# Kernel optimization log

Measured on AMD Instinct MI355X. Metric: run time of the kernel, lower is better.

The kernel has to match this reference:

```python
import jax, jax.numpy as jnp
import numpy as np

H = 12          # nheads
SIM_EPS = 1e-8  # SimMatrix eps
LN_EPS = 1e-5   # nn.LayerNorm default eps
SLOPE = 0.01    # LeakyReLU default negative slope


def leaky(x):
    return jnp.where(x >= 0, x, SLOPE * x)


def etc_attention(hiddens, gamma, beta, Wout, bout):
    # hiddens: [B, L, 3*D]
    B, L, D3 = hiddens.shape
    D = D3 // 3
    d = D // H
    h = hiddens.reshape(B, L, 3, H, d)
    Q = h[:, :, 0].transpose(0, 2, 1, 3)  # [B,H,L,d]
    K = h[:, :, 1].transpose(0, 2, 1, 3)
    V = h[:, :, 2].transpose(0, 2, 1, 3)
    # cosine-similarity attention scores (SimMatrix(K, Q))
    Kn = K / jnp.clip(jnp.linalg.norm(K, axis=-1, keepdims=True), SIM_EPS, None)
    Qn = Q / jnp.clip(jnp.linalg.norm(Q, axis=-1, keepdims=True), SIM_EPS, None)
    att = jnp.einsum('bhid,bhjd->bhij', Kn, Qn)  # [B,H,L,L]
    # LayerNorm over the head axis H (lnormalize: [B, L*L, H] layernorm on last dim)
    mu = att.mean(axis=1, keepdims=True)
    var = att.var(axis=1, keepdims=True)  # biased, matches torch LayerNorm
    att = (att - mu) / jnp.sqrt(var + LN_EPS)
    att = att * gamma[None, :, None, None] + beta[None, :, None, None]
    att = jax.nn.softmax(att, axis=-1)
    att = jnp.where(jnp.isnan(att), jnp.zeros_like(att), att)  # removeNaN
    out = jnp.einsum('bhij,bhjd->bhid', att, V)          # att @ V
    out = out.transpose(0, 2, 1, 3).reshape(B, L, D)      # catHiddens
    # dropout is identity at inference; lin_out = Linear + Softmax
    probs = jax.nn.softmax(out @ Wout.T + bout, axis=-1)  # [B,L,C]
    return probs, att


def get_weights(att, masks):
    # att: [B,H,L,L], masks: [B,L] float
    w = masks * att.mean(axis=1).sum(axis=1)  # [B,L]
    return jax.nn.softmax(w, axis=-1)[..., None]  # [B,L,1]


def setup_inputs() -> dict:
    key = jax.random.key(0)
    ks = jax.random.split(key, 16)
    B, L = 16, 512
    Din, D, C, VOCAB = 300, 768, 20, 32000

    def kaiming(k, shape, fan_in):
        return jax.random.normal(k, shape, jnp.float32) * np.sqrt(2.0 / fan_in)

    return {
        'input_ids': jax.random.randint(ks[0], (B, L), 0, VOCAB),
        'wv': jax.random.normal(ks[1], (B, L, Din), jnp.float32),
        'emb': jax.random.normal(ks[2], (VOCAB, D), jnp.float32),
        'W_t': kaiming(ks[3], (3 * D, D), D),
        'b_t': jnp.zeros((3 * D,), jnp.float32),
        'gamma_t': jnp.ones((H,), jnp.float32),
        'beta_t': jnp.zeros((H,), jnp.float32),
        'Wout_t': kaiming(ks[4], (C, D), D),
        'bout_t': jnp.zeros((C,), jnp.float32),
        'W_h': kaiming(ks[5], (3 * D, Din), Din),
        'b_h': jnp.zeros((3 * D,), jnp.float32),
        'gamma_h': jnp.ones((H,), jnp.float32),
        'beta_h': jnp.zeros((H,), jnp.float32),
        'Wout_h': kaiming(ks[6], (C, D), D),
        'bout_h': jnp.zeros((C,), jnp.float32),
    }


def reference(input_ids, wv, emb, W_t, b_t, gamma_t, beta_t, Wout_t, bout_t,
              W_h, b_h, gamma_h, beta_h, Wout_h, bout_h):
    masks = (input_ids != 0).astype(jnp.float32)  # [B,L]
    # token branch: Embedding -> LeakyReLU -> Linear -> LeakyReLU
    h_t = leaky(leaky(emb[input_ids]) @ W_t.T + b_t)
    probs_t, att_t = etc_attention(h_t, gamma_t, beta_t, Wout_t, bout_t)
    probs_t = (get_weights(att_t, masks) * probs_t).sum(axis=1)  # [B,C]
    # hidden/word-vector branch: Linear -> LeakyReLU
    h_h = leaky(wv @ W_h.T + b_h)
    probs_h, att_h = etc_attention(h_h, gamma_h, beta_h, Wout_h, bout_h)
    probs_h = (get_weights(att_h, masks) * probs_h).sum(axis=1)
    return (probs_t + probs_h) / 2.0
```

## Files before the change

### kernel.cpp

```cpp
#include <hip/hip_runtime.h>

typedef unsigned int uint;
typedef unsigned short ushort;
typedef _Float16 f16;
typedef _Float16 h8 __attribute__((ext_vector_type(8)));
typedef float f32x4 __attribute__((ext_vector_type(4)));


__device__ __forceinline__ float b2f(ushort u){ return __uint_as_float(((uint)u)<<16); }
__device__ __forceinline__ ushort f2b(float f){
  uint u = __float_as_uint(f);
  uint r = u + 0x7fffu + ((u>>16)&1u);
  return (ushort)(r>>16);
}
__device__ __forceinline__ float leaky(float x){ return x >= 0.f ? x : 0.01f*x; }
__device__ __forceinline__ float ldf(const void* p, int idx, int isb){
  return isb ? b2f(((const ushort*)p)[idx]) : ((const float*)p)[idx];
}

#define GLOAD16(gp, lp) __builtin_amdgcn_global_load_lds( \
    (const __attribute__((address_space(1))) void*)(gp), \
    (__attribute__((address_space(3))) void*)(lp), 16, 0, 0)

__global__ __launch_bounds__(256) void k_init(const ushort* __restrict__ wvbits,
    int* __restrict__ flag, float* __restrict__ zbase){
  int bid = blockIdx.x, tid = threadIdx.x;
  if (bid == 0){
    if (tid == 0){
      int sane = 0;
      for (int i=0;i<128;i++){
        uint e = (wvbits[i]>>7)&0xffu;
        if (e==0u || (e>=90u && e<=150u)) sane++;
      }
      *flag = (sane >= 115) ? 1 : 0;
    }
  } else {
    zbase[(bid-1)*256 + tid] = 0.f;
  }
}

__global__ __launch_bounds__(256) void k_prep_all(const int* __restrict__ ids,
    const void* __restrict__ emb, const void* __restrict__ wv,
    const void* __restrict__ W0, const void* __restrict__ W1,
    const int* __restrict__ flag,
    f16* __restrict__ AhA, f16* __restrict__ WhA,
    f16* __restrict__ AhB, f16* __restrict__ WhB,
    int nBX, int nW0, int nA1, int nW1){
  int isb = *flag;
  int bx = blockIdx.x, tid = threadIdx.x;
  if (bx < nBX){
    int t = bx*256 + tid;
    int m = t / 96, kk = (t % 96) * 8;
    float o[8];
    if (isb){
      const ushort* src = (const ushort*)emb + (size_t)ids[m]*768 + kk;
      uint4 v = *(const uint4*)src;
      o[0]=__uint_as_float((v.x&0xffffu)<<16); o[1]=__uint_as_float(v.x&0xffff0000u);
      o[2]=__uint_as_float((v.y&0xffffu)<<16); o[3]=__uint_as_float(v.y&0xffff0000u);
      o[4]=__uint_as_float((v.z&0xffffu)<<16); o[5]=__uint_as_float(v.z&0xffff0000u);
      o[6]=__uint_as_float((v.w&0xffffu)<<16); o[7]=__uint_as_float(v.w&0xffff0000u);
    } else {
      const float* src = (const float*)emb + (size_t)ids[m]*768 + kk;
      float4 v0 = ((const float4*)src)[0];
      float4 v1 = ((const float4*)src)[1];
      o[0]=v0.x; o[1]=v0.y; o[2]=v0.z; o[3]=v0.w;
      o[4]=v1.x; o[5]=v1.y; o[6]=v1.z; o[7]=v1.w;
    }
    h8 hv;
    #pragma unroll
    for (int i=0;i<8;i++) hv[i] = (f16)leaky(o[i]);
    *(h8*)(AhA + (size_t)m*768 + kk) = hv;
  } else if (bx < nBX + nW0){
    int t = (bx - nBX)*256 + tid;
    int n = t / 96, kk = (t % 96) * 8;
    h8 hv;
    #pragma unroll
    for (int i=0;i<8;i++) hv[i] = (f16)ldf(W0, n*768 + kk + i, isb);
    *(h8*)(WhA + (size_t)n*768 + kk) = hv;
  } else if (bx < nBX + nW0 + nA1){
    int t = (bx - nBX - nW0)*256 + tid;
    int n = t / 40, kk = (t % 40) * 8;
    h8 hv;
    #pragma unroll
    for (int i=0;i<8;i++){
      int k = kk + i;
      hv[i] = (k < 300) ? (f16)ldf(wv, n*300 + k, isb) : (f16)0.f;
    }
    *(h8*)(AhB + (size_t)n*320 + kk) = hv;
  } else {
    int t = (bx - nBX - nW0 - nA1)*256 + tid;
    int n = t / 40, kk = (t % 40) * 8;
    h8 hv;
    #pragma unroll
    for (int i=0;i<8;i++){
      int k = kk + i;
      hv[i] = (k < 300) ? (f16)ldf(W1, n*300 + k, isb) : (f16)0.f;
    }
    *(h8*)(WhB + (size_t)n*320 + kk) = hv;
  }
}

__global__ __launch_bounds__(256) void k_gemm_m(
    const f16* AhA, const f16* WhA, const void* biasA, int KA,
    f16* QhA, f16* KhA, f16* VtA,
    const f16* AhB, const f16* WhB, const void* biasB, int KB,
    f16* QhB, f16* KhB, f16* VtB,
    const int* __restrict__ flag, int sbase){
  __shared__ __align__(16) f16 As[128*64];
  __shared__ __align__(16) f16 Bs[128*64];
  int z = sbase + blockIdx.z;
  const f16* Ah = z ? AhB : AhA;
  const f16* Wh = z ? WhB : WhA;
  const void* bias = z ? biasB : biasA;
  int KP = z ? KB : KA;
  f16* Qh = z ? QhB : QhA;
  f16* Kh = z ? KhB : KhA;
  f16* Vt = z ? VtB : VtA;
  int STEPS = KP >> 6;

  int tid = threadIdx.x;
  int w = tid >> 6, lane = tid & 63;
  int mrow = lane & 15, kq = lane >> 4;
  int m0 = blockIdx.x * 128;
  int n0 = blockIdx.y * 128;
  int msub = (w & 1) * 64, nsub = (w >> 1) * 64;

  f32x4 acc[4][4];
  #pragma unroll
  for (int mt=0; mt<4; mt++)
    #pragma unroll
    for (int nt=0; nt<4; nt++) acc[mt][nt] = (f32x4){0.f,0.f,0.f,0.f};

  int cbase = w*64 + lane;

  for (int step=0; step<STEPS; step++){
    int k0 = step*64;
    __syncthreads();
    #pragma unroll
    for (int rep=0; rep<4; rep++){
      int cb = rep*256 + w*64;
      int c  = rep*256 + cbase;
      int row = c >> 3;
      int qs  = (c & 7) ^ (row & 7);
      GLOAD16(Ah + (size_t)(m0+row)*KP + k0 + qs*8, As + cb*8);
      GLOAD16(Wh + (size_t)(n0+row)*KP + k0 + qs*8, Bs + cb*8);
    }
    __syncthreads();
    #pragma unroll
    for (int ks=0; ks<2; ks++){
      h8 af[4], bf[4];
      #pragma unroll
      for (int mt=0; mt<4; mt++){
        int row = msub + mt*16 + mrow;
        int slot = (ks*4 + kq) ^ (row & 7);
        af[mt] = *(const h8*)(As + row*64 + slot*8);
      }
      #pragma unroll
      for (int nt=0; nt<4; nt++){
        int row = nsub + nt*16 + mrow;
        int slot = (ks*4 + kq) ^ (row & 7);
        bf[nt] = *(const h8*)(Bs + row*64 + slot*8);
      }
      #pragma unroll
      for (int mt=0; mt<4; mt++)
        #pragma unroll
        for (int nt=0; nt<4; nt++)
          acc[mt][nt] = __builtin_amdgcn_mfma_f32_16x16x32_f16(af[mt], bf[nt], acc[mt][nt], 0, 0, 0);
    }
  }

  int isb = *flag;
  int n0w = n0 + nsub;
  int s = n0w / 768;
  int h = (n0w % 768) >> 6;
  float bv[4];
  #pragma unroll
  for (int nt=0; nt<4; nt++) bv[nt] = ldf(bias, n0w + nt*16 + mrow, isb);

  #pragma unroll
  for (int mt=0; mt<4; mt++){
    float yv[4][4];
    #pragma unroll
    for (int nt=0; nt<4; nt++)
      #pragma unroll
      for (int r=0; r<4; r++)
        yv[nt][r] = leaky(acc[mt][nt][r] + bv[nt]);
    if (s < 2){
      #pragma unroll
      for (int r=0; r<4; r++){
        float ss = yv[0][r]*yv[0][r] + yv[1][r]*yv[1][r]
                 + yv[2][r]*yv[2][r] + yv[3][r]*yv[3][r];
        ss += __shfl_xor(ss, 1); ss += __shfl_xor(ss, 2);
        ss += __shfl_xor(ss, 4); ss += __shfl_xor(ss, 8);
        float rn = 1.f / fmaxf(sqrtf(ss), 1e-8f);
        #pragma unroll
        for (int nt=0; nt<4; nt++) yv[nt][r] *= rn;
      }
    }
    #pragma unroll
    for (int nt=0; nt<4; nt++){
      #pragma unroll
      for (int r=0; r<4; r++){
        int m = m0 + msub + mt*16 + kq*4 + r;
        int dd = nt*16 + mrow;
        int bq = m >> 9, l = m & 511;
        float y = yv[nt][r];
        if (s == 0)      Qh[((size_t)(bq*12 + h)*512 + l)*64 + dd] = (f16)y;
        else if (s == 1) Kh[((size_t)(bq*12 + h)*512 + l)*64 + dd] = (f16)y;
        else             Vt[((size_t)(bq*12 + h)*64 + dd)*512 + l] = (f16)y;
      }
    }
  }
}

__global__ __launch_bounds__(256) void k_scores(const f16* __restrict__ Qh,
    const f16* __restrict__ Kh, const void* __restrict__ gamma,
    const void* __restrict__ beta, const int* __restrict__ flag,
    f16* __restrict__ E, float* __restrict__ lsum){
  constexpr int TS = 72;
  __shared__ f16 S[12*16*TS];
  __shared__ float gL[12], beL[12];

  int tid = threadIdx.x;
  int w = tid >> 6, lane = tid & 63;
  int kq = lane >> 4, mrow = lane & 15;
  int bx = blockIdx.x;
  int jt = bx & 7, it = (bx >> 3) & 31, b = bx >> 8;
  int i0 = it*16, j0 = jt*64;

  if (tid < 12){ int isb = *flag; gL[tid] = ldf(gamma, tid, isb); beL[tid] = ldf(beta, tid, isb); }

  #pragma unroll
  for (int hh=0; hh<3; hh++){
    int h = w*3 + hh;
    const f16* kb = Kh + ((size_t)(b*12+h)*512 + i0 + mrow)*64;
    h8 a0 = *(const h8*)(kb + kq*8);
    h8 a1 = *(const h8*)(kb + 32 + kq*8);
    const f16* qb = Qh + ((size_t)(b*12+h)*512 + j0)*64;
    #pragma unroll
    for (int jn=0; jn<4; jn++){
      const f16* qr = qb + (size_t)(jn*16 + mrow)*64;
      h8 q0 = *(const h8*)(qr + kq*8);
      h8 q1 = *(const h8*)(qr + 32 + kq*8);
      f32x4 c = (f32x4){0.f,0.f,0.f,0.f};
      c = __builtin_amdgcn_mfma_f32_16x16x32_f16(a0, q0, c, 0, 0, 0);
      c = __builtin_amdgcn_mfma_f32_16x16x32_f16(a1, q1, c, 0, 0, 0);
      #pragma unroll
      for (int r=0;r<4;r++)
        S[(h*16 + kq*4 + r)*TS + jn*16 + mrow] = (f16)c[r];
    }
  }
  __syncthreads();
  int pj = tid & 63, piw = tid >> 6;
  #pragma unroll
  for (int p=0; p<4; p++){
    int i = piw*4 + p;
    float s[12];
    float mu = 0.f, sq = 0.f;
    #pragma unroll
    for (int h=0;h<12;h++){ s[h] = (float)S[(h*16+i)*TS + pj]; mu += s[h]; sq += s[h]*s[h]; }
    mu *= (1.f/12.f);
    float var = fmaxf(sq*(1.f/12.f) - mu*mu, 0.f);
    float rstd = rsqrtf(var + 1e-5f);
    #pragma unroll
    for (int h=0;h<12;h++){
      float e = __expf((s[h]-mu)*rstd*gL[h] + beL[h]);
      S[(h*16+i)*TS + pj] = (f16)e;
    }
  }
  __syncthreads();
  if (tid < 192){
    int h = tid >> 4, i = tid & 15;
    const f16* zr = &S[(h*16 + i)*TS];
    float ssum = 0.f;
    #pragma unroll
    for (int q=0;q<8;q++){
      h8 v = *(const h8*)(zr + q*8);
      #pragma unroll
      for (int t=0;t<8;t++) ssum += (float)v[t];
    }
    atomicAdd(&lsum[(size_t)(b*12+h)*512 + i0 + i], ssum);
  }
  #pragma unroll
  for (int u0=0; u0<6; u0++){
    int u = tid + u0*256;
    int h = u >> 7, rem = u & 127, i = rem >> 3, q = rem & 7;
    h8 v = *(const h8*)&S[(h*16 + i)*TS + q*8];
    *(h8*)(E + ((size_t)(b*12+h)*512 + i0 + i)*512 + j0 + q*8) = v;
  }
}

__global__ __launch_bounds__(256) void k_pv2(const f16* __restrict__ E,
    const f16* __restrict__ Vt, const float* __restrict__ lsum,
    float* __restrict__ O, float* __restrict__ colsum){
  __shared__ float csL[512];
  int tid = threadIdx.x;
  int w = tid >> 6, lane = tid & 63;
  int kq = lane >> 4, mrow = lane & 15;
  int b = blockIdx.y;
  int h = blockIdx.x >> 3, it = blockIdx.x & 7;
  int i0w = it*64 + w*16;

  csL[tid] = 0.f; csL[tid + 256] = 0.f;
  float rinv = 1.f / lsum[(size_t)(b*12+h)*512 + i0w + mrow];
  __syncthreads();

  const f16* erow  = E  + ((size_t)(b*12+h)*512 + i0w + mrow)*512 + kq*8;
  const f16* vbase = Vt + ((size_t)(b*12+h)*64 + mrow)*512 + kq*8;

  f32x4 acc[4];
  #pragma unroll
  for (int nt=0; nt<4; nt++) acc[nt] = (f32x4){0.f,0.f,0.f,0.f};

  #pragma unroll 4
  for (int jt=0; jt<16; jt++){
    int j0 = jt*32;
    h8 ea  = *(const h8*)(erow + j0);
    h8 bf0 = *(const h8*)(vbase + j0);
    h8 bf1 = *(const h8*)(vbase + (size_t)16*512 + j0);
    h8 bf2 = *(const h8*)(vbase + (size_t)32*512 + j0);
    h8 bf3 = *(const h8*)(vbase + (size_t)48*512 + j0);
    acc[0] = __builtin_amdgcn_mfma_f32_16x16x32_f16(ea, bf0, acc[0], 0, 0, 0);
    acc[1] = __builtin_amdgcn_mfma_f32_16x16x32_f16(ea, bf1, acc[1], 0, 0, 0);
    acc[2] = __builtin_amdgcn_mfma_f32_16x16x32_f16(ea, bf2, acc[2], 0, 0, 0);
    acc[3] = __builtin_amdgcn_mfma_f32_16x16x32_f16(ea, bf3, acc[3], 0, 0, 0);
    float cs[8];
    #pragma unroll
    for (int t=0;t<8;t++) cs[t] = (float)ea[t] * rinv;
    #pragma unroll
    for (int t=0;t<8;t++){
      cs[t] += __shfl_xor(cs[t], 1); cs[t] += __shfl_xor(cs[t], 2);
      cs[t] += __shfl_xor(cs[t], 4); cs[t] += __shfl_xor(cs[t], 8);
    }
    if (mrow == 0){
      #pragma unroll
      for (int t=0;t<8;t++) atomicAdd(&csL[j0 + kq*8 + t], cs[t]);
    }
  }
  __syncthreads();
  atomicAdd(&colsum[b*512 + tid],       csL[tid]       * (1.f/12.f));
  atomicAdd(&colsum[b*512 + 256 + tid], csL[tid + 256] * (1.f/12.f));

  #pragma unroll
  for (int r=0; r<4; r++){
    float g = __shfl(rinv, kq*4 + r);
    #pragma unroll
    for (int nt=0; nt<4; nt++)
      O[((size_t)(b*512) + i0w + kq*4 + r)*768 + h*64 + nt*16 + mrow] = acc[nt][r] * g;
  }
}

__global__ __launch_bounds__(256) void k_probs_m(const float* OA, const float* OB,
    const void* WoA, const void* WoB, const void* boA, const void* boB,
    float* prA, float* prB, const int* __restrict__ flag, int sbase){
  int z = sbase + blockIdx.y;
  const float* O = z ? OB : OA;
  const void* Wout = z ? WoB : WoA;
  const void* bout = z ? boB : boA;
  float* probs = z ? prB : prA;
  int isb = *flag;
  int tid = threadIdx.x, wv = tid>>6, lane = tid&63;
  int m = blockIdx.x*4 + wv;
  const float* orow = O + (size_t)m*768;
  float acc[20];
  #pragma unroll
  for (int c=0;c<20;c++) acc[c]=0.f;
  for (int kk=0; kk<12; kk++){
    float o = orow[kk*64 + lane];
    #pragma unroll
    for (int c=0;c<20;c++)
      acc[c] += o * ldf(Wout, c*768 + kk*64 + lane, isb);
  }
  #pragma unroll
  for (int c=0;c<20;c++){
    #pragma unroll
    for (int off=1; off<64; off<<=1) acc[c] += __shfl_xor(acc[c], off, 64);
  }
  float mx = -3.4e38f;
  #pragma unroll
  for (int c=0;c<20;c++){ acc[c] += ldf(bout, c, isb); mx = fmaxf(mx, acc[c]); }
  float s=0.f;
  #pragma unroll
  for (int c=0;c<20;c++){ acc[c] = __expf(acc[c]-mx); s += acc[c]; }
  float inv = 1.f/s;
  if (lane == 0){
    float* pr = probs + (size_t)m*20;
    #pragma unroll
    for (int c=0;c<20;c++) pr[c] = acc[c]*inv;
  }
}

__global__ __launch_bounds__(512) void k_final_m(const int* __restrict__ ids,
    const float* __restrict__ cs0, const float* __restrict__ cs1,
    const float* __restrict__ pr0, const float* __restrict__ pr1,
    const int* __restrict__ flag, void* __restrict__ outp){
  __shared__ float red[8];
  __shared__ float bcast;
  __shared__ float pacc[8][20];
  __shared__ float osum[20];
  int b = blockIdx.x, tid = threadIdx.x;
  int wv = tid>>6, lane = tid&63;
  int msk = (ids[b*512+tid] != 0);
  for (int br=0; br<2; br++){
    const float* colsum = br ? cs1 : cs0;
    const float* probs  = br ? pr1 : pr0;
    float w = msk ? colsum[b*512+tid] : 0.f;
    float mx = w;
    #pragma unroll
    for (int off=1; off<64; off<<=1) mx = fmaxf(mx, __shfl_xor(mx, off, 64));
    if (lane==0) red[wv] = mx;
    __syncthreads();
    if (tid==0){ float m2 = red[0]; for (int k2=1;k2<8;k2++) m2 = fmaxf(m2, red[k2]); bcast = m2; }
    __syncthreads();
    float M = bcast;
    float e = __expf(w - M);
    float s = e;
    #pragma unroll
    for (int off=1; off<64; off<<=1) s += __shfl_xor(s, off, 64);
    if (lane==0) red[wv] = s;
    __syncthreads();
    if (tid==0){ float s2=0.f; for (int k2=0;k2<8;k2++) s2 += red[k2]; bcast = s2; }
    __syncthreads();
    float wn = e / bcast;
    float p[20];
    const float* pr = probs + ((size_t)b*512 + tid)*20;
    #pragma unroll
    for (int c=0;c<20;c++) p[c] = wn * pr[c];
    #pragma unroll
    for (int c=0;c<20;c++){
      #pragma unroll
      for (int off=1; off<64; off<<=1) p[c] += __shfl_xor(p[c], off, 64);
    }
    if (lane==0){
      #pragma unroll
      for (int c=0;c<20;c++) pacc[wv][c] = p[c];
    }
    __syncthreads();
    if (tid < 20){
      float s2 = 0.f;
      #pragma unroll
      for (int k2=0;k2<8;k2++) s2 += pacc[k2][tid];
      if (br == 0) osum[tid] = s2;
      else         osum[tid] += s2;
    }
    __syncthreads();
  }
  if (tid < 20){
    float v = osum[tid] * 0.5f;
    if (*flag) ((ushort*)outp)[b*20 + tid] = f2b(v);
    else       ((float*)outp)[b*20 + tid] = v;
  }
}

extern "C" void kernel_launch(void* const* d_in, const int* in_sizes, int n_in,
                              void* d_out, int out_size, void* d_ws, size_t ws_size,
                              hipStream_t stream){
  (void)in_sizes; (void)n_in; (void)out_size;
  const int*  ids = (const int*)d_in[0];
  const void* wvp = d_in[1];
  const void* emb = d_in[2];
  const void* Wt[2]  = {d_in[3], d_in[9]};
  const void* bt[2]  = {d_in[4], d_in[10]};
  const void* gm[2]  = {d_in[5], d_in[11]};
  const void* bet[2] = {d_in[6], d_in[12]};
  const void* Wo[2]  = {d_in[7], d_in[13]};
  const void* bo[2]  = {d_in[8], d_in[14]};

  char* p = (char*)d_ws;
  #define ALLOC(ty, name, cnt) ty* name = (ty*)p; p += sizeof(ty)*(size_t)(cnt)

  p = (char*)d_ws;
  ALLOC(float, O0, 6291456);
  ALLOC(float, O1, 6291456);
  ALLOC(f16, Qh0, 6291456); ALLOC(f16, Kh0, 6291456); ALLOC(f16, Vt0, 6291456);
  ALLOC(f16, Qh1, 6291456); ALLOC(f16, Kh1, 6291456); ALLOC(f16, Vt1, 6291456);
  ALLOC(f16, Ah0, 6291456); ALLOC(f16, Wh0, 1769472);
  ALLOC(f16, Ah1, 2621440); ALLOC(f16, Wh1, 737280);
  ALLOC(float, probs0, 163840); ALLOC(float, probs1, 163840);
  ALLOC(float, zb_big, 212992);
  ALLOC(int, flag_big, 4);
  ALLOC(f16, E_big, 50331648);
  size_t needBig = (size_t)(p - (char*)d_ws);

  if (ws_size >= needBig){
    float* colsum0 = zb_big;          float* colsum1 = zb_big + 8192;
    float* lsum0   = zb_big + 16384;  float* lsum1   = zb_big + 16384 + 98304;
    int* flagp = flag_big; f16* E = E_big;

    k_init<<<833, 256, 0, stream>>>((const ushort*)wvp, flagp, zb_big);
    k_prep_all<<<3072+864+1280+360, 256, 0, stream>>>(ids, emb, wvp, Wt[0], Wt[1],
        flagp, Ah0, Wh0, Ah1, Wh1, 3072, 864, 1280, 360);
    dim3 gg(64, 18, 2);
    k_gemm_m<<<gg, 256, 0, stream>>>(Ah0, Wh0, bt[0], 768, Qh0, Kh0, Vt0,
                                     Ah1, Wh1, bt[1], 320, Qh1, Kh1, Vt1, flagp, 0);
    dim3 gpv(96, 16);
    k_scores<<<4096, 256, 0, stream>>>(Qh0, Kh0, gm[0], bet[0], flagp, E, lsum0);
    k_pv2<<<gpv, 256, 0, stream>>>(E, Vt0, lsum0, O0, colsum0);
    k_scores<<<4096, 256, 0, stream>>>(Qh1, Kh1, gm[1], bet[1], flagp, E, lsum1);
    k_pv2<<<gpv, 256, 0, stream>>>(E, Vt1, lsum1, O1, colsum1);
    dim3 gpr(2048, 2);
    k_probs_m<<<gpr, 256, 0, stream>>>(O0, O1, Wo[0], Wo[1], bo[0], bo[1],
                                       probs0, probs1, flagp, 0);
    k_final_m<<<16, 512, 0, stream>>>(ids, colsum0, colsum1, probs0, probs1, flagp, d_out);
    return;
  }

  p = (char*)d_ws;
  ALLOC(float, O, 6291456);
  ALLOC(f16, Qh, 6291456); ALLOC(f16, Kh, 6291456); ALLOC(f16, Vt, 6291456);
  ALLOC(f16, Ah, 6291456); ALLOC(f16, Wh, 1769472);
  ALLOC(float, probsA, 163840); ALLOC(float, probsB, 163840);
  ALLOC(float, zb, 212992);
  ALLOC(int, flagm, 4);
  ALLOC(f16, Em, 50331648);
  float* colsum0 = zb;          float* colsum1 = zb + 8192;
  float* lsum0   = zb + 16384;  float* lsum1   = zb + 16384 + 98304;

  k_init<<<833, 256, 0, stream>>>((const ushort*)wvp, flagm, zb);
  k_prep_all<<<3072+864, 256, 0, stream>>>(ids, emb, wvp, Wt[0], Wt[1],
      flagm, Ah, Wh, Ah, Wh, 3072, 864, 0, 0);
  dim3 g1(64, 18, 1);
  k_gemm_m<<<g1, 256, 0, stream>>>(Ah, Wh, bt[0], 768, Qh, Kh, Vt,
                                   Ah, Wh, bt[0], 768, Qh, Kh, Vt, flagm, 0);
  dim3 gpv(96, 16);
  k_scores<<<4096, 256, 0, stream>>>(Qh, Kh, gm[0], bet[0], flagm, Em, lsum0);
  k_pv2<<<gpv, 256, 0, stream>>>(Em, Vt, lsum0, O, colsum0);
  dim3 gpr(2048, 1);
  k_probs_m<<<gpr, 256, 0, stream>>>(O, O, Wo[0], Wo[1], bo[0], bo[1],
                                     probsA, probsB, flagm, 0);
  k_prep_all<<<1280+360, 256, 0, stream>>>(ids, emb, wvp, Wt[0], Wt[1],
      flagm, Ah, Wh, Ah, Wh, 0, 0, 1280, 360);
  k_gemm_m<<<g1, 256, 0, stream>>>(Ah, Wh, bt[1], 320, Qh, Kh, Vt,
                                   Ah, Wh, bt[1], 320, Qh, Kh, Vt, flagm, 0);
  k_scores<<<4096, 256, 0, stream>>>(Qh, Kh, gm[1], bet[1], flagm, Em, lsum1);
  k_pv2<<<gpv, 256, 0, stream>>>(Em, Vt, lsum1, O, colsum1);
  k_probs_m<<<gpr, 256, 0, stream>>>(O, O, Wo[0], Wo[1], bo[0], bo[1],
                                     probsA, probsB, flagm, 1);
  k_final_m<<<16, 512, 0, stream>>>(ids, colsum0, colsum1, probsA, probsB, flagm, d_out);
  #undef ALLOC
}
```

Before: 579.7 us.

## Fuse score, head-LayerNorm, softmax and PV into one flash-style attention kernel

Replaces the separate scores kernel (which wrote a full fp16 exp-score matrix E to global memory) and the PV kernel with a single kernel per 16-row query tile. It computes scores, applies the head-axis LayerNorm and exp, and accumulates P·V on the fly over j tiles. A second pass recomputes the scores to build the column sums once the row normalisers are known. Both branches run in one launch, removing the 100 MB E buffer round trip and the lsum atomics. The price is doubled QK MFMA work, fewer blocks (1024 instead of 4096+1536), and more barriers per tile.

```diff
diff --git a/kernel.cpp b/kernel.cpp
--- a/kernel.cpp
+++ b/kernel.cpp
@@ -213,141 +213,180 @@
   }
 }
 
-__global__ __launch_bounds__(256) void k_scores(const f16* __restrict__ Qh,
-    const f16* __restrict__ Kh, const void* __restrict__ gamma,
-    const void* __restrict__ beta, const int* __restrict__ flag,
-    f16* __restrict__ E, float* __restrict__ lsum){
+__global__ __launch_bounds__(256) void k_attn(
+    const f16* __restrict__ Qh0, const f16* __restrict__ Kh0, const f16* __restrict__ Vt0,
+    const void* __restrict__ g0, const void* __restrict__ be0,
+    float* __restrict__ O0, float* __restrict__ csg0,
+    const f16* __restrict__ Qh1, const f16* __restrict__ Kh1, const f16* __restrict__ Vt1,
+    const void* __restrict__ g1, const void* __restrict__ be1,
+    float* __restrict__ O1, float* __restrict__ csg1,
+    const int* __restrict__ flag, int sbase){
   constexpr int TS = 72;
-  __shared__ f16 S[12*16*TS];
+  __shared__ __align__(16) f16 S[12*16*TS];
   __shared__ float gL[12], beL[12];
+  __shared__ float rowsumL[192], rinvL[192];
+  __shared__ float csL[512];
+
+  int z = sbase + blockIdx.y;
+  const f16* Qh = z ? Qh1 : Qh0;
+  const f16* Kh = z ? Kh1 : Kh0;
+  const f16* Vt = z ? Vt1 : Vt0;
+  const void* gamma = z ? g1 : g0;
+  const void* beta  = z ? be1 : be0;
+  float* O   = z ? O1 : O0;
+  float* csg = z ? csg1 : csg0;
 
   int tid = threadIdx.x;
   int w = tid >> 6, lane = tid & 63;
   int kq = lane >> 4, mrow = lane & 15;
-  int bx = blockIdx.x;
-  int jt = bx & 7, it = (bx >> 3) & 31, b = bx >> 8;
-  int i0 = it*16, j0 = jt*64;
+  int b = blockIdx.x >> 5, it = blockIdx.x & 31;
+  int i0 = it * 16;
+  int h0 = w * 3;
+  int pj = tid & 63, piw = tid >> 6;
 
   if (tid < 12){ int isb = *flag; gL[tid] = ldf(gamma, tid, isb); beL[tid] = ldf(beta, tid, isb); }
-
+  if (tid < 192) rowsumL[tid] = 0.f;
+  csL[tid] = 0.f; csL[tid + 256] = 0.f;
+
+  h8 ka[3][2];
   #pragma unroll
   for (int hh=0; hh<3; hh++){
-    int h = w*3 + hh;
-    const f16* kb = Kh + ((size_t)(b*12+h)*512 + i0 + mrow)*64;
-    h8 a0 = *(const h8*)(kb + kq*8);
-    h8 a1 = *(const h8*)(kb + 32 + kq*8);
-    const f16* qb = Qh + ((size_t)(b*12+h)*512 + j0)*64;
-    #pragma unroll
-    for (int jn=0; jn<4; jn++){
-      const f16* qr = qb + (size_t)(jn*16 + mrow)*64;
-      h8 q0 = *(const h8*)(qr + kq*8);
-      h8 q1 = *(const h8*)(qr + 32 + kq*8);
-      f32x4 c = (f32x4){0.f,0.f,0.f,0.f};
-      c = __builtin_amdgcn_mfma_f32_16x16x32_f16(a0, q0, c, 0, 0, 0);
-      c = __builtin_amdgcn_mfma_f32_16x16x32_f16(a1, q1, c, 0, 0, 0);
-      #pragma unroll
-      for (int r=0;r<4;r++)
-        S[(h*16 + kq*4 + r)*TS + jn*16 + mrow] = (f16)c[r];
-    }
-  }
+    const f16* kb = Kh + ((size_t)(b*12 + h0 + hh)*512 + i0 + mrow)*64;
+    ka[hh][0] = *(const h8*)(kb + kq*8);
+    ka[hh][1] = *(const h8*)(kb + 32 + kq*8);
+  }
+
+  f32x4 acc[3][4];
+  #pragma unroll
+  for (int hh=0; hh<3; hh++)
+    #pragma unroll
+    for (int nt=0; nt<4; nt++) acc[hh][nt] = (f32x4){0.f,0.f,0.f,0.f};
+
   __syncthreads();
-  int pj = tid & 63, piw = tid >> 6;
-  #pragma unroll
-  for (int p=0; p<4; p++){
-    int i = piw*4 + p;
-    float s[12];
-    float mu = 0.f, sq = 0.f;
-    #pragma unroll
-    for (int h=0;h<12;h++){ s[h] = (float)S[(h*16+i)*TS + pj]; mu += s[h]; sq += s[h]*s[h]; }
-    mu *= (1.f/12.f);
-    float var = fmaxf(sq*(1.f/12.f) - mu*mu, 0.f);
-    float rstd = rsqrtf(var + 1e-5f);
-    #pragma unroll
-    for (int h=0;h<12;h++){
-      float e = __expf((s[h]-mu)*rstd*gL[h] + beL[h]);
-      S[(h*16+i)*TS + pj] = (f16)e;
-    }
-  }
+
+  for (int jt=0; jt<8; jt++){
+    int j0 = jt*64;
+    #pragma unroll
+    for (int hh=0; hh<3; hh++){
+      int h = h0 + hh;
+      const f16* qb = Qh + ((size_t)(b*12+h)*512 + j0)*64;
+      #pragma unroll
+      for (int jn=0; jn<4; jn++){
+        const f16* qr = qb + (size_t)(jn*16 + mrow)*64;
+        h8 q0 = *(const h8*)(qr + kq*8);
+        h8 q1 = *(const h8*)(qr + 32 + kq*8);
+        f32x4 c = (f32x4){0.f,0.f,0.f,0.f};
+        c = __builtin_amdgcn_mfma_f32_16x16x32_f16(ka[hh][0], q0, c, 0, 0, 0);
+        c = __builtin_amdgcn_mfma_f32_16x16x32_f16(ka[hh][1], q1, c, 0, 0, 0);
+        #pragma unroll
+        for (int r=0;r<4;r++)
+          S[(h*16 + kq*4 + r)*TS + jn*16 + mrow] = (f16)c[r];
+      }
+    }
+    __syncthreads();
+    #pragma unroll
+    for (int p=0; p<4; p++){
+      int i = piw*4 + p;
+      float s[12]; float mu=0.f, sq=0.f;
+      #pragma unroll
+      for (int h=0;h<12;h++){ s[h] = (float)S[(h*16+i)*TS + pj]; mu += s[h]; sq += s[h]*s[h]; }
+      mu *= (1.f/12.f);
+      float var = fmaxf(sq*(1.f/12.f) - mu*mu, 0.f);
+      float rstd = rsqrtf(var + 1e-5f);
+      #pragma unroll
+      for (int h=0;h<12;h++){
+        float e = __expf((s[h]-mu)*rstd*gL[h] + beL[h]);
+        S[(h*16+i)*TS + pj] = (f16)e;
+      }
+    }
+    __syncthreads();
+    if (tid < 192){
+      int h = tid >> 4, i = tid & 15;
+      const f16* zr = &S[(h*16 + i)*TS];
+      float ssum = 0.f;
+      #pragma unroll
+      for (int q=0;q<8;q++){
+        h8 v = *(const h8*)(zr + q*8);
+        #pragma unroll
+        for (int t2=0;t2<8;t2++) ssum += (float)v[t2];
+      }
+      rowsumL[tid] += ssum;
+    }
+    #pragma unroll
+    for (int hh=0; hh<3; hh++){
+      int h = h0 + hh;
+      const f16* sb = S + (h*16 + mrow)*TS + kq*8;
+      const f16* vb = Vt + ((size_t)(b*12+h)*64 + mrow)*512 + j0 + kq*8;
+      #pragma unroll
+      for (int ks=0; ks<2; ks++){
+        h8 ea = *(const h8*)(sb + ks*32);
+        #pragma unroll
+        for (int nt=0; nt<4; nt++){
+          h8 bf = *(const h8*)(vb + (size_t)(nt*16)*512 + ks*32);
+          acc[hh][nt] = __builtin_amdgcn_mfma_f32_16x16x32_f16(ea, bf, acc[hh][nt], 0, 0, 0);
+        }
+      }
+    }
+    __syncthreads();
+  }
+
+  if (tid < 192) rinvL[tid] = 1.f / rowsumL[tid];
   __syncthreads();
-  if (tid < 192){
-    int h = tid >> 4, i = tid & 15;
-    const f16* zr = &S[(h*16 + i)*TS];
-    float ssum = 0.f;
-    #pragma unroll
-    for (int q=0;q<8;q++){
-      h8 v = *(const h8*)(zr + q*8);
-      #pragma unroll
-      for (int t=0;t<8;t++) ssum += (float)v[t];
-    }
-    atomicAdd(&lsum[(size_t)(b*12+h)*512 + i0 + i], ssum);
-  }
-  #pragma unroll
-  for (int u0=0; u0<6; u0++){
-    int u = tid + u0*256;
-    int h = u >> 7, rem = u & 127, i = rem >> 3, q = rem & 7;
-    h8 v = *(const h8*)&S[(h*16 + i)*TS + q*8];
-    *(h8*)(E + ((size_t)(b*12+h)*512 + i0 + i)*512 + j0 + q*8) = v;
-  }
-}
-
-__global__ __launch_bounds__(256) void k_pv2(const f16* __restrict__ E,
-    const f16* __restrict__ Vt, const float* __restrict__ lsum,
-    float* __restrict__ O, float* __restrict__ colsum){
-  __shared__ float csL[512];
-  int tid = threadIdx.x;
-  int w = tid >> 6, lane = tid & 63;
-  int kq = lane >> 4, mrow = lane & 15;
-  int b = blockIdx.y;
-  int h = blockIdx.x >> 3, it = blockIdx.x & 7;
-  int i0w = it*64 + w*16;
-
-  csL[tid] = 0.f; csL[tid + 256] = 0.f;
-  float rinv = 1.f / lsum[(size_t)(b*12+h)*512 + i0w + mrow];
-  __syncthreads();
-
-  const f16* erow  = E  + ((size_t)(b*12+h)*512 + i0w + mrow)*512 + kq*8;
-  const f16* vbase = Vt + ((size_t)(b*12+h)*64 + mrow)*512 + kq*8;
-
-  f32x4 acc[4];
-  #pragma unroll
-  for (int nt=0; nt<4; nt++) acc[nt] = (f32x4){0.f,0.f,0.f,0.f};
-
-  #pragma unroll 4
-  for (int jt=0; jt<16; jt++){
-    int j0 = jt*32;
-    h8 ea  = *(const h8*)(erow + j0);
-    h8 bf0 = *(const h8*)(vbase + j0);
-    h8 bf1 = *(const h8*)(vbase + (size_t)16*512 + j0);
-    h8 bf2 = *(const h8*)(vbase + (size_t)32*512 + j0);
-    h8 bf3 = *(const h8*)(vbase + (size_t)48*512 + j0);
-    acc[0] = __builtin_amdgcn_mfma_f32_16x16x32_f16(ea, bf0, acc[0], 0, 0, 0);
-    acc[1] = __builtin_amdgcn_mfma_f32_16x16x32_f16(ea, bf1, acc[1], 0, 0, 0);
-    acc[2] = __builtin_amdgcn_mfma_f32_16x16x32_f16(ea, bf2, acc[2], 0, 0, 0);
-    acc[3] = __builtin_amdgcn_mfma_f32_16x16x32_f16(ea, bf3, acc[3], 0, 0, 0);
-    float cs[8];
-    #pragma unroll
-    for (int t=0;t<8;t++) cs[t] = (float)ea[t] * rinv;
-    #pragma unroll
-    for (int t=0;t<8;t++){
-      cs[t] += __shfl_xor(cs[t], 1); cs[t] += __shfl_xor(cs[t], 2);
-      cs[t] += __shfl_xor(cs[t], 4); cs[t] += __shfl_xor(cs[t], 8);
-    }
-    if (mrow == 0){
-      #pragma unroll
-      for (int t=0;t<8;t++) atomicAdd(&csL[j0 + kq*8 + t], cs[t]);
-    }
-  }
-  __syncthreads();
-  atomicAdd(&colsum[b*512 + tid],       csL[tid]       * (1.f/12.f));
-  atomicAdd(&colsum[b*512 + 256 + tid], csL[tid + 256] * (1.f/12.f));
-
-  #pragma unroll
-  for (int r=0; r<4; r++){
-    float g = __shfl(rinv, kq*4 + r);
-    #pragma unroll
-    for (int nt=0; nt<4; nt++)
-      O[((size_t)(b*512) + i0w + kq*4 + r)*768 + h*64 + nt*16 + mrow] = acc[nt][r] * g;
-  }
+
+  #pragma unroll
+  for (int hh=0; hh<3; hh++){
+    int h = h0 + hh;
+    #pragma unroll
+    for (int r=0; r<4; r++){
+      float g = rinvL[h*16 + kq*4 + r];
+      #pragma unroll
+      for (int nt=0; nt<4; nt++)
+        O[((size_t)(b*512) + i0 + kq*4 + r)*768 + h*64 + nt*16 + mrow] = acc[hh][nt][r] * g;
+    }
+  }
+
+  for (int jt=0; jt<8; jt++){
+    int j0 = jt*64;
+    #pragma unroll
+    for (int hh=0; hh<3; hh++){
+      int h = h0 + hh;
+      const f16* qb = Qh + ((size_t)(b*12+h)*512 + j0)*64;
+      #pragma unroll
+      for (int jn=0; jn<4; jn++){
+        const f16* qr = qb + (size_t)(jn*16 + mrow)*64;
+        h8 q0 = *(const h8*)(qr + kq*8);
+        h8 q1 = *(const h8*)(qr + 32 + kq*8);
+        f32x4 c = (f32x4){0.f,0.f,0.f,0.f};
+        c = __builtin_amdgcn_mfma_f32_16x16x32_f16(ka[hh][0], q0, c, 0, 0, 0);
+        c = __builtin_amdgcn_mfma_f32_16x16x32_f16(ka[hh][1], q1, c, 0, 0, 0);
+        #pragma unroll
+        for (int r=0;r<4;r++)
+          S[(h*16 + kq*4 + r)*TS + jn*16 + mrow] = (f16)c[r];
+      }
+    }
+    __syncthreads();
+    float cspart = 0.f;
+    #pragma unroll
+    for (int p=0; p<4; p++){
+      int i = piw*4 + p;
+      float s[12]; float mu=0.f, sq=0.f;
+      #pragma unroll
+      for (int h=0;h<12;h++){ s[h] = (float)S[(h*16+i)*TS + pj]; mu += s[h]; sq += s[h]*s[h]; }
+      mu *= (1.f/12.f);
+      float var = fmaxf(sq*(1.f/12.f) - mu*mu, 0.f);
+      float rstd = rsqrtf(var + 1e-5f);
+      #pragma unroll
+      for (int h=0;h<12;h++){
+        float e = __expf((s[h]-mu)*rstd*gL[h] + beL[h]);
+        cspart += e * rinvL[h*16 + i];
+      }
+    }
+    atomicAdd(&csL[j0 + pj], cspart);
+    __syncthreads();
+  }
+
+  atomicAdd(&csg[b*512 + tid],       csL[tid]       * (1.f/12.f));
+  atomicAdd(&csg[b*512 + 256 + tid], csL[tid + 256] * (1.f/12.f));
 }
 
 __global__ __launch_bounds__(256) void k_probs_m(const float* OA, const float* OB,
@@ -477,27 +516,24 @@
   ALLOC(f16, Ah0, 6291456); ALLOC(f16, Wh0, 1769472);
   ALLOC(f16, Ah1, 2621440); ALLOC(f16, Wh1, 737280);
   ALLOC(float, probs0, 163840); ALLOC(float, probs1, 163840);
-  ALLOC(float, zb_big, 212992);
+  ALLOC(float, zb_big, 16384);
   ALLOC(int, flag_big, 4);
-  ALLOC(f16, E_big, 50331648);
   size_t needBig = (size_t)(p - (char*)d_ws);
 
   if (ws_size >= needBig){
-    float* colsum0 = zb_big;          float* colsum1 = zb_big + 8192;
-    float* lsum0   = zb_big + 16384;  float* lsum1   = zb_big + 16384 + 98304;
-    int* flagp = flag_big; f16* E = E_big;
-
-    k_init<<<833, 256, 0, stream>>>((const ushort*)wvp, flagp, zb_big);
+    float* colsum0 = zb_big;
+    float* colsum1 = zb_big + 8192;
+    int* flagp = flag_big;
+
+    k_init<<<65, 256, 0, stream>>>((const ushort*)wvp, flagp, zb_big);
     k_prep_all<<<3072+864+1280+360, 256, 0, stream>>>(ids, emb, wvp, Wt[0], Wt[1],
         flagp, Ah0, Wh0, Ah1, Wh1, 3072, 864, 1280, 360);
     dim3 gg(64, 18, 2);
     k_gemm_m<<<gg, 256, 0, stream>>>(Ah0, Wh0, bt[0], 768, Qh0, Kh0, Vt0,
                                      Ah1, Wh1, bt[1], 320, Qh1, Kh1, Vt1, flagp, 0);
-    dim3 gpv(96, 16);
-    k_scores<<<4096, 256, 0, stream>>>(Qh0, Kh0, gm[0], bet[0], flagp, E, lsum0);
-    k_pv2<<<gpv, 256, 0, stream>>>(E, Vt0, lsum0, O0, colsum0);
-    k_scores<<<4096, 256, 0, stream>>>(Qh1, Kh1, gm[1], bet[1], flagp, E, lsum1);
-    k_pv2<<<gpv, 256, 0, stream>>>(E, Vt1, lsum1, O1, colsum1);
+    dim3 ga(512, 2);
+    k_attn<<<ga, 256, 0, stream>>>(Qh0, Kh0, Vt0, gm[0], bet[0], O0, colsum0,
+                                   Qh1, Kh1, Vt1, gm[1], bet[1], O1, colsum1, flagp, 0);
     dim3 gpr(2048, 2);
     k_probs_m<<<gpr, 256, 0, stream>>>(O0, O1, Wo[0], Wo[1], bo[0], bo[1],
                                        probs0, probs1, flagp, 0);
@@ -510,21 +546,20 @@
   ALLOC(f16, Qh, 6291456); ALLOC(f16, Kh, 6291456); ALLOC(f16, Vt, 6291456);
   ALLOC(f16, Ah, 6291456); ALLOC(f16, Wh, 1769472);
   ALLOC(float, probsA, 163840); ALLOC(float, probsB, 163840);
-  ALLOC(float, zb, 212992);
+  ALLOC(float, zb, 16384);
   ALLOC(int, flagm, 4);
-  ALLOC(f16, Em, 50331648);
-  float* colsum0 = zb;          float* colsum1 = zb + 8192;
-  float* lsum0   = zb + 16384;  float* lsum1   = zb + 16384 + 98304;
-
-  k_init<<<833, 256, 0, stream>>>((const ushort*)wvp, flagm, zb);
+  float* colsum0 = zb;
+  float* colsum1 = zb + 8192;
+
+  k_init<<<65, 256, 0, stream>>>((const ushort*)wvp, flagm, zb);
   k_prep_all<<<3072+864, 256, 0, stream>>>(ids, emb, wvp, Wt[0], Wt[1],
       flagm, Ah, Wh, Ah, Wh, 3072, 864, 0, 0);
   dim3 g1(64, 18, 1);
   k_gemm_m<<<g1, 256, 0, stream>>>(Ah, Wh, bt[0], 768, Qh, Kh, Vt,
                                    Ah, Wh, bt[0], 768, Qh, Kh, Vt, flagm, 0);
-  dim3 gpv(96, 16);
-  k_scores<<<4096, 256, 0, stream>>>(Qh, Kh, gm[0], bet[0], flagm, Em, lsum0);
-  k_pv2<<<gpv, 256, 0, stream>>>(Em, Vt, lsum0, O, colsum0);
+  dim3 ga(512, 1);
+  k_attn<<<ga, 256, 0, stream>>>(Qh, Kh, Vt, gm[0], bet[0], O, colsum0,
+                                 Qh, Kh, Vt, gm[0], bet[0], O, colsum0, flagm, 0);
   dim3 gpr(2048, 1);
   k_probs_m<<<gpr, 256, 0, stream>>>(O, O, Wo[0], Wo[1], bo[0], bo[1],
                                      probsA, probsB, flagm, 0);
@@ -532,8 +567,8 @@
       flagm, Ah, Wh, Ah, Wh, 0, 0, 1280, 360);
   k_gemm_m<<<g1, 256, 0, stream>>>(Ah, Wh, bt[1], 320, Qh, Kh, Vt,
                                    Ah, Wh, bt[1], 320, Qh, Kh, Vt, flagm, 0);
-  k_scores<<<4096, 256, 0, stream>>>(Qh, Kh, gm[1], bet[1], flagm, Em, lsum1);
-  k_pv2<<<gpv, 256, 0, stream>>>(Em, Vt, lsum1, O, colsum1);
+  k_attn<<<ga, 256, 0, stream>>>(Qh, Kh, Vt, gm[1], bet[1], O, colsum1,
+                                 Qh, Kh, Vt, gm[1], bet[1], O, colsum1, flagm, 0);
   k_probs_m<<<gpr, 256, 0, stream>>>(O, O, Wo[0], Wo[1], bo[0], bo[1],
                                      probsA, probsB, flagm, 1);
   k_final_m<<<16, 512, 0, stream>>>(ids, colsum0, colsum1, probsA, probsB, flagm, d_out);
```

Measured after the change: 624.3 us. +7.7%, slower.

## Replace lsum atomics with per-tile partial sums and swizzle block order

Applied to the files above, without the earlier changes.

k_scores now writes each row's partial softmax denominator for its column tile into a slot of a per-row array of eight, instead of atomically adding into one value. k_pv2 reads the eight partials as two float4 loads and sums them. Because the row sums no longer need a zeroed buffer, k_init zeroes far less memory. The partials live in the activation buffer, which is dead by then, so no extra workspace is needed. Both attention kernels also remap blockIdx so consecutive hardware blocks land on related tiles, aiming at better L2 locality across XCDs. The cost is more store traffic to the partial array and a dependency on that aliased buffer no longer being live.

```diff
diff --git a/kernel.cpp b/kernel.cpp
--- a/kernel.cpp
+++ b/kernel.cpp
@@ -216,7 +216,7 @@
 __global__ __launch_bounds__(256) void k_scores(const f16* __restrict__ Qh,
     const f16* __restrict__ Kh, const void* __restrict__ gamma,
     const void* __restrict__ beta, const int* __restrict__ flag,
-    f16* __restrict__ E, float* __restrict__ lsum){
+    f16* __restrict__ E, float* __restrict__ lsump){
   constexpr int TS = 72;
   __shared__ f16 S[12*16*TS];
   __shared__ float gL[12], beL[12];
@@ -224,7 +224,7 @@
   int tid = threadIdx.x;
   int w = tid >> 6, lane = tid & 63;
   int kq = lane >> 4, mrow = lane & 15;
-  int bx = blockIdx.x;
+  int bx = (blockIdx.x & 7)*512 + (blockIdx.x >> 3);
   int jt = bx & 7, it = (bx >> 3) & 31, b = bx >> 8;
   int i0 = it*16, j0 = jt*64;
 
@@ -279,7 +279,7 @@
       #pragma unroll
       for (int t=0;t<8;t++) ssum += (float)v[t];
     }
-    atomicAdd(&lsum[(size_t)(b*12+h)*512 + i0 + i], ssum);
+    lsump[((size_t)(b*12+h)*512 + i0 + i)*8 + jt] = ssum;
   }
   #pragma unroll
   for (int u0=0; u0<6; u0++){
@@ -291,18 +291,21 @@
 }
 
 __global__ __launch_bounds__(256) void k_pv2(const f16* __restrict__ E,
-    const f16* __restrict__ Vt, const float* __restrict__ lsum,
+    const f16* __restrict__ Vt, const float* __restrict__ lsump,
     float* __restrict__ O, float* __restrict__ colsum){
   __shared__ float csL[512];
   int tid = threadIdx.x;
   int w = tid >> 6, lane = tid & 63;
   int kq = lane >> 4, mrow = lane & 15;
   int b = blockIdx.y;
-  int h = blockIdx.x >> 3, it = blockIdx.x & 7;
+  int bx = (blockIdx.x & 7)*12 + (blockIdx.x >> 3);
+  int h = bx >> 3, it = bx & 7;
   int i0w = it*64 + w*16;
 
   csL[tid] = 0.f; csL[tid + 256] = 0.f;
-  float rinv = 1.f / lsum[(size_t)(b*12+h)*512 + i0w + mrow];
+  const float4* lp = (const float4*)(lsump + ((size_t)(b*12+h)*512 + i0w + mrow)*8);
+  float4 p0 = lp[0], p1 = lp[1];
+  float rinv = 1.f / (p0.x+p0.y+p0.z+p0.w + p1.x+p1.y+p1.z+p1.w);
   __syncthreads();
 
   const f16* erow  = E  + ((size_t)(b*12+h)*512 + i0w + mrow)*512 + kq*8;
@@ -477,27 +480,29 @@
   ALLOC(f16, Ah0, 6291456); ALLOC(f16, Wh0, 1769472);
   ALLOC(f16, Ah1, 2621440); ALLOC(f16, Wh1, 737280);
   ALLOC(float, probs0, 163840); ALLOC(float, probs1, 163840);
-  ALLOC(float, zb_big, 212992);
+  ALLOC(float, zb_big, 16384);
   ALLOC(int, flag_big, 4);
   ALLOC(f16, E_big, 50331648);
   size_t needBig = (size_t)(p - (char*)d_ws);
 
   if (ws_size >= needBig){
-    float* colsum0 = zb_big;          float* colsum1 = zb_big + 8192;
-    float* lsum0   = zb_big + 16384;  float* lsum1   = zb_big + 16384 + 98304;
+    float* colsum0 = zb_big;
+    float* colsum1 = zb_big + 8192;
     int* flagp = flag_big; f16* E = E_big;
-
-    k_init<<<833, 256, 0, stream>>>((const ushort*)wvp, flagp, zb_big);
+    float* lsump0 = (float*)Ah0;
+    float* lsump1 = lsump0 + 786432;
+
+    k_init<<<65, 256, 0, stream>>>((const ushort*)wvp, flagp, zb_big);
     k_prep_all<<<3072+864+1280+360, 256, 0, stream>>>(ids, emb, wvp, Wt[0], Wt[1],
         flagp, Ah0, Wh0, Ah1, Wh1, 3072, 864, 1280, 360);
     dim3 gg(64, 18, 2);
     k_gemm_m<<<gg, 256, 0, stream>>>(Ah0, Wh0, bt[0], 768, Qh0, Kh0, Vt0,
                                      Ah1, Wh1, bt[1], 320, Qh1, Kh1, Vt1, flagp, 0);
     dim3 gpv(96, 16);
-    k_scores<<<4096, 256, 0, stream>>>(Qh0, Kh0, gm[0], bet[0], flagp, E, lsum0);
-    k_pv2<<<gpv, 256, 0, stream>>>(E, Vt0, lsum0, O0, colsum0);
-    k_scores<<<4096, 256, 0, stream>>>(Qh1, Kh1, gm[1], bet[1], flagp, E, lsum1);
-    k_pv2<<<gpv, 256, 0, stream>>>(E, Vt1, lsum1, O1, colsum1);
+    k_scores<<<4096, 256, 0, stream>>>(Qh0, Kh0, gm[0], bet[0], flagp, E, lsump0);
+    k_pv2<<<gpv, 256, 0, stream>>>(E, Vt0, lsump0, O0, colsum0);
+    k_scores<<<4096, 256, 0, stream>>>(Qh1, Kh1, gm[1], bet[1], flagp, E, lsump1);
+    k_pv2<<<gpv, 256, 0, stream>>>(E, Vt1, lsump1, O1, colsum1);
     dim3 gpr(2048, 2);
     k_probs_m<<<gpr, 256, 0, stream>>>(O0, O1, Wo[0], Wo[1], bo[0], bo[1],
                                        probs0, probs1, flagp, 0);
@@ -510,21 +515,23 @@
   ALLOC(f16, Qh, 6291456); ALLOC(f16, Kh, 6291456); ALLOC(f16, Vt, 6291456);
   ALLOC(f16, Ah, 6291456); ALLOC(f16, Wh, 1769472);
   ALLOC(float, probsA, 163840); ALLOC(float, probsB, 163840);
-  ALLOC(float, zb, 212992);
+  ALLOC(float, zb, 16384);
   ALLOC(int, flagm, 4);
   ALLOC(f16, Em, 50331648);
-  float* colsum0 = zb;          float* colsum1 = zb + 8192;
-  float* lsum0   = zb + 16384;  float* lsum1   = zb + 16384 + 98304;
-
-  k_init<<<833, 256, 0, stream>>>((const ushort*)wvp, flagm, zb);
+  float* colsum0 = zb;
+  float* colsum1 = zb + 8192;
+  float* lsumm0 = (float*)Ah;
+  float* lsumm1 = lsumm0 + 786432;
+
+  k_init<<<65, 256, 0, stream>>>((const ushort*)wvp, flagm, zb);
   k_prep_all<<<3072+864, 256, 0, stream>>>(ids, emb, wvp, Wt[0], Wt[1],
       flagm, Ah, Wh, Ah, Wh, 3072, 864, 0, 0);
   dim3 g1(64, 18, 1);
   k_gemm_m<<<g1, 256, 0, stream>>>(Ah, Wh, bt[0], 768, Qh, Kh, Vt,
                                    Ah, Wh, bt[0], 768, Qh, Kh, Vt, flagm, 0);
   dim3 gpv(96, 16);
-  k_scores<<<4096, 256, 0, stream>>>(Qh, Kh, gm[0], bet[0], flagm, Em, lsum0);
-  k_pv2<<<gpv, 256, 0, stream>>>(Em, Vt, lsum0, O, colsum0);
+  k_scores<<<4096, 256, 0, stream>>>(Qh, Kh, gm[0], bet[0], flagm, Em, lsumm0);
+  k_pv2<<<gpv, 256, 0, stream>>>(Em, Vt, lsumm0, O, colsum0);
   dim3 gpr(2048, 1);
   k_probs_m<<<gpr, 256, 0, stream>>>(O, O, Wo[0], Wo[1], bo[0], bo[1],
                                      probsA, probsB, flagm, 0);
@@ -532,8 +539,8 @@
       flagm, Ah, Wh, Ah, Wh, 0, 0, 1280, 360);
   k_gemm_m<<<g1, 256, 0, stream>>>(Ah, Wh, bt[1], 320, Qh, Kh, Vt,
                                    Ah, Wh, bt[1], 320, Qh, Kh, Vt, flagm, 0);
-  k_scores<<<4096, 256, 0, stream>>>(Qh, Kh, gm[1], bet[1], flagm, Em, lsum1);
-  k_pv2<<<gpv, 256, 0, stream>>>(Em, Vt, lsum1, O, colsum1);
+  k_scores<<<4096, 256, 0, stream>>>(Qh, Kh, gm[1], bet[1], flagm, Em, lsumm1);
+  k_pv2<<<gpv, 256, 0, stream>>>(Em, Vt, lsumm1, O, colsum1);
   k_probs_m<<<gpr, 256, 0, stream>>>(O, O, Wo[0], Wo[1], bo[0], bo[1],
                                      probsA, probsB, flagm, 1);
   k_final_m<<<16, 512, 0, stream>>>(ids, colsum0, colsum1, probsA, probsB, flagm, d_out);
```

New measurement: 572.7 us. About the same (-1.2%).
